# Kernel tuning notes

Hardware: AMD Instinct MI355X
Metric: run time of the kernel (lower is better)

Reference implementation:

```python
import jax, jax.numpy as jnp
import numpy as np

N_EV, N_CS, N_TR, N_ENV = 40000, 30000, 20000, 10000
N = N_EV + N_CS + N_TR + N_ENV  # 100000 nodes
E = 3_200_000                   # edges (avg degree 32)
FEAT, HID = 32, 64
N_GRAPHS, NPG = 100, 1000       # 100 graphs of 1000 nodes


def _p(k, shape, scale=0.1):
    return (jax.random.normal(k, shape, jnp.float32) * scale)


def setup_inputs() -> dict:
    key = jax.random.key(0)
    ks = jax.random.split(key, 24)
    inp = {
        'ev_features': jax.random.normal(ks[0], (N_EV, 6), jnp.float32),
        'cs_features': jax.random.normal(ks[1], (N_CS, 4), jnp.float32),
        'tr_features': jax.random.normal(ks[2], (N_TR, 2), jnp.float32),
        'env_features': jax.random.normal(ks[3], (N_ENV, 5), jnp.float32),
        'edge_index': jax.random.randint(ks[4], (2, E), 0, N, jnp.int32),
        'ev_indexes': jnp.arange(0, N_EV, dtype=jnp.int32),
        'cs_indexes': jnp.arange(N_EV, N_EV + N_CS, dtype=jnp.int32),
        'tr_indexes': jnp.arange(N_EV + N_CS, N_EV + N_CS + N_TR, dtype=jnp.int32),
        'env_indexes': jnp.arange(N - N_ENV, N, dtype=jnp.int32),
        'batch': (jnp.arange(N, dtype=jnp.int32) // NPG),
        'W_ev': _p(ks[5], (6, FEAT)),  'b_ev': _p(ks[6], (FEAT,)),
        'W_cs': _p(ks[7], (4, FEAT)),  'b_cs': _p(ks[8], (FEAT,)),
        'W_tr': _p(ks[9], (2, FEAT)),  'b_tr': _p(ks[10], (FEAT,)),
        'W_env': _p(ks[11], (5, FEAT)), 'b_env': _p(ks[12], (FEAT,)),
        'W1': _p(ks[13], (FEAT, HID)),      'b1': _p(ks[14], (HID,)),
        'W2': _p(ks[15], (HID, 2 * HID)),   'b2': _p(ks[16], (2 * HID,)),
        'W3': _p(ks[17], (2 * HID, HID)),   'b3': _p(ks[18], (HID,)),
    }
    return inp


def gcn_conv(x, src, dst, W, b):
    # PyG GCNConv: h = x W; add self-loops; symmetric norm D^-1/2 (A+I) D^-1/2; + bias
    h = x @ W
    ones_e = jnp.ones((src.shape[0],), h.dtype)
    deg = jnp.ones((N,), h.dtype).at[dst].add(ones_e)  # includes self-loop weight 1
    dinv = jax.lax.rsqrt(deg)
    norm = dinv[src] * dinv[dst]                       # [E]
    out = (h * (dinv * dinv)[:, None]).at[dst].add(h[src] * norm[:, None])
    return out + b


def reference(ev_features, cs_features, tr_features, env_features,
              edge_index, ev_indexes, cs_indexes, tr_indexes, env_indexes, batch,
              W_ev, b_ev, W_cs, b_cs, W_tr, b_tr, W_env, b_env,
              W1, b1, W2, b2, W3, b3):
    src, dst = edge_index[0], edge_index[1]
    x = jnp.zeros((N, FEAT), jnp.float32)
    x = x.at[ev_indexes].set(ev_features @ W_ev + b_ev)
    x = x.at[cs_indexes].set(cs_features @ W_cs + b_cs)
    x = x.at[tr_indexes].set(tr_features @ W_tr + b_tr)
    x = x.at[env_indexes].set(env_features @ W_env + b_env)

    x1 = gcn_conv(x, src, dst, W1, b1)                 # [N, HID]
    h = jax.nn.relu(x1)
    h = jax.nn.relu(gcn_conv(h, src, dst, W2, b2))     # [N, 2*HID]
    h = jax.nn.relu(gcn_conv(h, src, dst, W3, b3))     # [N, HID]
    h = h + x1                                          # residual

    # global_mean_pool over graph segments
    sums = jax.ops.segment_sum(h, batch, num_segments=N_GRAPHS)
    cnts = jax.ops.segment_sum(jnp.ones((N,), h.dtype), batch, num_segments=N_GRAPHS)
    return sums / cnts[:, None]
```

## Files before the change

### kernel.cpp

```cpp
#include <hip/hip_runtime.h>
#include <hip/hip_bf16.h>


#define THREADS 256
#define BINSHIFT 8
#define EPBA 4096
#define SCANCH 8

typedef __attribute__((ext_vector_type(8))) short short8;
typedef __attribute__((ext_vector_type(4))) float f32x4;

__device__ __forceinline__ unsigned bfpack2(float lo, float hi) {
    unsigned ul = __float_as_uint(lo);
    unsigned uh = __float_as_uint(hi);
    ul = (ul + 0x7fffu + ((ul >> 16) & 1u)) >> 16;
    uh = (uh + 0x7fffu + ((uh >> 16) & 1u)) & 0xffff0000u;
    return ul | uh;
}

__device__ __forceinline__ void bfacc(uint2 v, float& a0, float& a1,
                                      float& a2, float& a3) {
    a0 += __uint_as_float(v.x << 16);
    a1 += __uint_as_float(v.x & 0xffff0000u);
    a2 += __uint_as_float(v.y << 16);
    a3 += __uint_as_float(v.y & 0xffff0000u);
}

__device__ __forceinline__ short8 as_short8(uint4 u) {
    union { uint4 u; short8 s; } c; c.u = u; return c.s;
}

__global__ __launch_bounds__(THREADS)
void k_partcnt(const int* __restrict__ dst, int* __restrict__ counts,
               int nblk_part, int nb, int e) {
    extern __shared__ int h[];
    int t = threadIdx.x;
    for (int i = t; i < nb; i += THREADS) h[i] = 0;
    __syncthreads();
    int lo = blockIdx.x * EPBA;
    int hi = min(lo + EPBA, e);
    for (int i = lo + t; i < hi; i += THREADS)
        atomicAdd(&h[dst[i] >> BINSHIFT], 1);
    __syncthreads();
    for (int i = t; i < nb; i += THREADS)
        counts[(size_t)i * nblk_part + blockIdx.x] = h[i];
}

__global__ __launch_bounds__(THREADS)
void k_scanrows(int* __restrict__ counts, int* __restrict__ bintot, int nblk_part) {
    __shared__ int wsum[THREADS];
    int* row = counts + (size_t)blockIdx.x * nblk_part;
    int t = threadIdx.x;
    int base = t * SCANCH;
    int v[SCANCH];
    int s = 0;
#pragma unroll
    for (int k = 0; k < SCANCH; ++k) {
        v[k] = (base + k < nblk_part) ? row[base + k] : 0;
        s += v[k];
    }
    wsum[t] = s;
    __syncthreads();
    for (int off = 1; off < THREADS; off <<= 1) {
        int a = (t >= off) ? wsum[t - off] : 0;
        __syncthreads();
        wsum[t] += a;
        __syncthreads();
    }
    int run = wsum[t] - s;
#pragma unroll
    for (int k = 0; k < SCANCH; ++k) {
        int c = v[k];
        if (base + k < nblk_part) row[base + k] = run;
        run += c;
    }
    if (t == THREADS - 1) bintot[blockIdx.x] = run;
}

__global__ __launch_bounds__(512)
void k_binscan(const int* __restrict__ bintot, int* __restrict__ binptr,
               int nb, int e) {
    __shared__ int lds[512];
    int t = threadIdx.x;
    int v = (t < nb) ? bintot[t] : 0;
    lds[t] = v;
    __syncthreads();
    for (int off = 1; off < 512; off <<= 1) {
        int a = (t >= off) ? lds[t - off] : 0;
        __syncthreads();
        lds[t] += a;
        __syncthreads();
    }
    if (t < nb) binptr[t] = lds[t] - v;
    if (t == 0) binptr[nb] = e;
}

__global__ __launch_bounds__(THREADS)
void k_partwrite(const int* __restrict__ src, const int* __restrict__ dst,
                 const int* __restrict__ binptr, const int* __restrict__ counts,
                 int nblk_part, unsigned* __restrict__ pairs, int nb, int e) {
    extern __shared__ int smem[];
    int* base = smem;
    int* cnt  = smem + nb;
    int t = threadIdx.x;
    for (int i = t; i < nb; i += THREADS) {
        base[i] = binptr[i] + counts[(size_t)i * nblk_part + blockIdx.x];
        cnt[i] = 0;
    }
    __syncthreads();
    int lo = blockIdx.x * EPBA;
    int hi = min(lo + EPBA, e);
    for (int i = lo + t; i < hi; i += THREADS) {
        int s = src[i], d = dst[i];
        int b = d >> BINSHIFT;
        int pos = atomicAdd(&cnt[b], 1);
        pairs[base[b] + pos] = ((unsigned)s << BINSHIFT) | (unsigned)(d & ((1 << BINSHIFT) - 1));
    }
}

__global__ __launch_bounds__(THREADS)
void k_bincsr(const unsigned* __restrict__ pairs, const int* __restrict__ binptr,
              int* __restrict__ rowptr, float* __restrict__ dinv,
              int* __restrict__ srcs, int n, int nb, int e) {
    __shared__ int lcnt[256];
    __shared__ int lofs[256];
    int b = blockIdx.x, t = threadIdx.x;
    int e0 = binptr[b], e1 = binptr[b + 1];
    int n0 = b << BINSHIFT;
    constexpr unsigned NMASK = (1u << BINSHIFT) - 1u;
    lcnt[t] = 0;
    __syncthreads();
    for (int j = e0 + t; j < e1; j += THREADS)
        atomicAdd(&lcnt[pairs[j] & NMASK], 1);
    __syncthreads();
    int c = lcnt[t];
    lofs[t] = c;
    __syncthreads();
    for (int off = 1; off < THREADS; off <<= 1) {
        int a = (t >= off) ? lofs[t - off] : 0;
        __syncthreads();
        lofs[t] += a;
        __syncthreads();
    }
    int excl = lofs[t] - c;
    __syncthreads();
    lofs[t] = excl;
    int node = n0 + t;
    if (node < n) {
        rowptr[node] = e0 + excl;
        dinv[node] = rsqrtf((float)c + 1.0f);
    }
    if (b == nb - 1 && t == 0) rowptr[n] = e;
    __syncthreads();
    for (int j = e0 + t; j < e1; j += THREADS) {
        unsigned pp = pairs[j];
        int pos = e0 + atomicAdd(&lofs[pp & NMASK], 1);
        srcs[pos] = (int)(pp >> BINSHIFT);
    }
}

template <int K>
__global__ __launch_bounds__(THREADS)
void k_embed(const float* __restrict__ f, const float* __restrict__ W,
             const float* __restrict__ b, const int* __restrict__ idx,
             const float* __restrict__ dinv, int rows, unsigned* __restrict__ xb) {
    int g = blockIdx.x * THREADS + threadIdx.x;
    int r = g >> 4, cp = g & 15;
    if (r >= rows) return;
    int node = idx[r];
    float dv = dinv[node];
    float a0 = b[2 * cp], a1 = b[2 * cp + 1];
#pragma unroll
    for (int k = 0; k < K; ++k) {
        float fv = f[r * K + k];
        a0 += fv * W[k * 32 + 2 * cp];
        a1 += fv * W[k * 32 + 2 * cp + 1];
    }
    xb[(size_t)node * 16 + cp] = bfpack2(dv * a0, dv * a1);
}

template <bool HASBIAS, bool OUTRELU, bool HASRES, bool OUTBF>
__global__ __launch_bounds__(THREADS)
void k_gather64(const unsigned* __restrict__ tblb, const int* __restrict__ rowptr,
                const int* __restrict__ srcs, const float* __restrict__ dinv,
                const float* __restrict__ bias, const unsigned* __restrict__ resid,
                void* __restrict__ outp, int n) {
    int gt = blockIdx.x * THREADS + threadIdx.x;
    int node = gt >> 6;
    int lane = threadIdx.x & 63;
    if (node >= n) return;
    int qw = lane >> 4, li = lane & 15;
    const uint2* t2 = reinterpret_cast<const uint2*>(tblb);
    float a0 = 0.f, a1 = 0.f, a2 = 0.f, a3 = 0.f;
    int beg = rowptr[node], end = rowptr[node + 1];
    int j = beg;
    for (; j + 16 <= end; j += 16) {
        int i0 = srcs[j + qw];
        int i1 = srcs[j + 4 + qw];
        int i2 = srcs[j + 8 + qw];
        int i3 = srcs[j + 12 + qw];
        uint2 v0 = t2[(size_t)i0 * 16 + li];
        uint2 v1 = t2[(size_t)i1 * 16 + li];
        uint2 v2 = t2[(size_t)i2 * 16 + li];
        uint2 v3 = t2[(size_t)i3 * 16 + li];
        bfacc(v0, a0, a1, a2, a3);
        bfacc(v1, a0, a1, a2, a3);
        bfacc(v2, a0, a1, a2, a3);
        bfacc(v3, a0, a1, a2, a3);
    }
    for (; j + 8 <= end; j += 8) {
        int i0 = srcs[j + qw];
        int i1 = srcs[j + 4 + qw];
        uint2 v0 = t2[(size_t)i0 * 16 + li];
        uint2 v1 = t2[(size_t)i1 * 16 + li];
        bfacc(v0, a0, a1, a2, a3);
        bfacc(v1, a0, a1, a2, a3);
    }
    int rem = end - j;
    if (qw < rem) {
        uint2 v = t2[(size_t)srcs[j + qw] * 16 + li];
        bfacc(v, a0, a1, a2, a3);
    }
    if (qw + 4 < rem) {
        uint2 v = t2[(size_t)srcs[j + 4 + qw] * 16 + li];
        bfacc(v, a0, a1, a2, a3);
    }
    a0 += __shfl_down(a0, 32, 64); a1 += __shfl_down(a1, 32, 64);
    a2 += __shfl_down(a2, 32, 64); a3 += __shfl_down(a3, 32, 64);
    a0 += __shfl_down(a0, 16, 64); a1 += __shfl_down(a1, 16, 64);
    a2 += __shfl_down(a2, 16, 64); a3 += __shfl_down(a3, 16, 64);
    if (lane < 16) {
        uint2 sv = t2[(size_t)node * 16 + li];
        bfacc(sv, a0, a1, a2, a3);
        float dv = dinv[node];
        float r0 = dv * a0, r1 = dv * a1, r2 = dv * a2, r3 = dv * a3;
        if (HASBIAS) {
            float4 bv = *reinterpret_cast<const float4*>(bias + 4 * li);
            r0 += bv.x; r1 += bv.y; r2 += bv.z; r3 += bv.w;
        }
        if (OUTRELU) {
            r0 = fmaxf(r0, 0.f); r1 = fmaxf(r1, 0.f);
            r2 = fmaxf(r2, 0.f); r3 = fmaxf(r3, 0.f);
        }
        if (HASRES) {
            uint2 rv = reinterpret_cast<const uint2*>(resid)[(size_t)node * 16 + li];
            bfacc(rv, r0, r1, r2, r3);
        }
        if (OUTBF) {
            uint2 o = {bfpack2(r0, r1), bfpack2(r2, r3)};
            reinterpret_cast<uint2*>(outp)[(size_t)node * 16 + li] = o;
        } else {
            float4 o = {r0, r1, r2, r3};
            reinterpret_cast<float4*>(outp)[(size_t)node * 16 + li] = o;
        }
    }
}

__global__ __launch_bounds__(THREADS)
void k_gather32(const unsigned* __restrict__ tblb, const int* __restrict__ rowptr,
                const int* __restrict__ srcs, const float* __restrict__ dinv,
                unsigned* __restrict__ outb, int n) {
    int gt = blockIdx.x * THREADS + threadIdx.x;
    int node = gt >> 6;
    int lane = threadIdx.x & 63;
    if (node >= n) return;
    int og = lane >> 3, li = lane & 7;
    const uint2* t2 = reinterpret_cast<const uint2*>(tblb);
    float a0 = 0.f, a1 = 0.f, a2 = 0.f, a3 = 0.f;
    int beg = rowptr[node], end = rowptr[node + 1];
    int j = beg;
    for (; j + 16 <= end; j += 16) {
        int i0 = srcs[j + og];
        int i1 = srcs[j + 8 + og];
        uint2 v0 = t2[(size_t)i0 * 8 + li];
        uint2 v1 = t2[(size_t)i1 * 8 + li];
        bfacc(v0, a0, a1, a2, a3);
        bfacc(v1, a0, a1, a2, a3);
    }
    for (; j + 8 <= end; j += 8) {
        int i0 = srcs[j + og];
        uint2 v0 = t2[(size_t)i0 * 8 + li];
        bfacc(v0, a0, a1, a2, a3);
    }
    int rem = end - j;
    if (og < rem) {
        uint2 v = t2[(size_t)srcs[j + og] * 8 + li];
        bfacc(v, a0, a1, a2, a3);
    }
    a0 += __shfl_down(a0, 32, 64); a1 += __shfl_down(a1, 32, 64);
    a2 += __shfl_down(a2, 32, 64); a3 += __shfl_down(a3, 32, 64);
    a0 += __shfl_down(a0, 16, 64); a1 += __shfl_down(a1, 16, 64);
    a2 += __shfl_down(a2, 16, 64); a3 += __shfl_down(a3, 16, 64);
    a0 += __shfl_down(a0, 8, 64);  a1 += __shfl_down(a1, 8, 64);
    a2 += __shfl_down(a2, 8, 64);  a3 += __shfl_down(a3, 8, 64);
    if (lane < 8) {
        uint2 sv = t2[(size_t)node * 8 + li];
        bfacc(sv, a0, a1, a2, a3);
        float dv = dinv[node];
        uint2 o = {bfpack2(dv * a0, dv * a1), bfpack2(dv * a2, dv * a3)};
        reinterpret_cast<uint2*>(outb)[(size_t)node * 8 + li] = o;
    }
}

template <int FIN, int FOUT>
__global__ __launch_bounds__(THREADS)
void k_wprep(const float* __restrict__ W, unsigned* __restrict__ Wtb) {
    int g = blockIdx.x * THREADS + threadIdx.x;
    if (g >= FOUT * (FIN / 2)) return;
    int nn = g / (FIN / 2), kq = g % (FIN / 2);
    float lo = W[(size_t)(2 * kq) * FOUT + nn];
    float hi = W[(size_t)(2 * kq + 1) * FOUT + nn];
    Wtb[g] = bfpack2(lo, hi);
}

template <int FIN, int FOUT, int EXTRA>
__global__ __launch_bounds__(THREADS)
void k_mmfa(const unsigned* __restrict__ xinb, const unsigned* __restrict__ wtb,
            const float* __restrict__ bias, const float* __restrict__ dinv,
            unsigned* __restrict__ outb, unsigned* __restrict__ outb2, int nrows) {
    constexpr int FH = FIN / 2;
    constexpr int KS = FIN / 32;
    constexpr int MT = FOUT / 16;
    int tid = threadIdx.x;
    int lane = tid & 63;
    int lg = lane >> 4, li = lane & 15;
    int node = blockIdx.x * 64 + (tid >> 6) * 16 + li;
    int nc = min(node, nrows - 1);

    const uint4* xr = reinterpret_cast<const uint4*>(xinb + (size_t)nc * FH);
    short8 bf[KS];
#pragma unroll
    for (int ks = 0; ks < KS; ++ks) bf[ks] = as_short8(xr[ks * 4 + lg]);

    f32x4 acc[MT];
#pragma unroll
    for (int mt = 0; mt < MT; ++mt) acc[mt] = (f32x4){0.f, 0.f, 0.f, 0.f};

#pragma unroll
    for (int ks = 0; ks < KS; ++ks) {
#pragma unroll
        for (int mt = 0; mt < MT; ++mt) {
            uint4 wu = *reinterpret_cast<const uint4*>(
                wtb + (size_t)(mt * 16 + li) * FH + ks * 16 + lg * 4);
            acc[mt] = __builtin_amdgcn_mfma_f32_16x16x32_bf16(
                as_short8(wu), bf[ks], acc[mt], 0, 0, 0);
        }
    }

    if (node >= nrows) return;
    float dv = (EXTRA != 3) ? dinv[node] : 0.f;
#pragma unroll
    for (int mt = 0; mt < MT; ++mt) {
        float v0 = acc[mt][0], v1 = acc[mt][1], v2 = acc[mt][2], v3 = acc[mt][3];
        int m0 = mt * 16 + lg * 4;
        if (EXTRA == 1 || EXTRA == 3) {
            float4 bv = *reinterpret_cast<const float4*>(bias + m0);
            v0 += bv.x; v1 += bv.y; v2 += bv.z; v3 += bv.w;
        }
        size_t ob = (size_t)node * (FOUT / 2) + mt * 8 + lg * 2;
        if (EXTRA == 1) {
            uint2 o = {bfpack2(v0, v1), bfpack2(v2, v3)};
            *reinterpret_cast<uint2*>(outb + ob) = o;
            uint2 s = {bfpack2(dv * fmaxf(v0, 0.f), dv * fmaxf(v1, 0.f)),
                       bfpack2(dv * fmaxf(v2, 0.f), dv * fmaxf(v3, 0.f))};
            *reinterpret_cast<uint2*>(outb2 + ob) = s;
        }
        if (EXTRA == 3) {
            uint2 o = {bfpack2(fmaxf(v0, 0.f), fmaxf(v1, 0.f)),
                       bfpack2(fmaxf(v2, 0.f), fmaxf(v3, 0.f))};
            *reinterpret_cast<uint2*>(outb + ob) = o;
        }
        if (EXTRA == 2) {
            uint2 o = {bfpack2(dv * v0, dv * v1), bfpack2(dv * v2, dv * v3)};
            *reinterpret_cast<uint2*>(outb + ob) = o;
        }
    }
}

__global__ __launch_bounds__(THREADS)
void k_pool(const float* __restrict__ h, const int* __restrict__ batch,
            float* __restrict__ sums, float* __restrict__ cnts, int n) {
    int c = threadIdx.x & 63;
    int rq = threadIdx.x >> 6;
    int r0 = blockIdx.x * THREADS;
    int rend = min(r0 + THREADS, n);
    int curg = -1;
    float acc = 0.f, cacc = 0.f;
    for (int r = r0 + rq; r < rend; r += 4) {
        int g = batch[r];
        if (g != curg) {
            if (curg >= 0) {
                atomicAdd(&sums[(size_t)curg * 64 + c], acc);
                if (c == 0) atomicAdd(&cnts[curg], cacc);
            }
            curg = g; acc = 0.f; cacc = 0.f;
        }
        acc += h[(size_t)r * 64 + c];
        cacc += 1.f;
    }
    if (curg >= 0) {
        atomicAdd(&sums[(size_t)curg * 64 + c], acc);
        if (c == 0) atomicAdd(&cnts[curg], cacc);
    }
}

__global__ __launch_bounds__(THREADS)
void k_div(const float* __restrict__ sums, const float* __restrict__ cnts,
           float* __restrict__ out, int total) {
    int i = blockIdx.x * THREADS + threadIdx.x;
    if (i < total) out[i] = sums[i] / cnts[i >> 6];
}

static inline size_t alignup(size_t v) { return (v + 255) & ~(size_t)255; }

extern "C" void kernel_launch(void* const* d_in, const int* in_sizes, int n_in,
                              void* d_out, int out_size, void* d_ws, size_t ws_size,
                              hipStream_t stream) {
    const float* ev_f  = (const float*)d_in[0];
    const float* cs_f  = (const float*)d_in[1];
    const float* tr_f  = (const float*)d_in[2];
    const float* env_f = (const float*)d_in[3];
    const int*   ei    = (const int*)d_in[4];
    const int*   ev_i  = (const int*)d_in[5];
    const int*   cs_i  = (const int*)d_in[6];
    const int*   tr_i  = (const int*)d_in[7];
    const int*   env_i = (const int*)d_in[8];
    const int*   batch = (const int*)d_in[9];
    const float* W_ev = (const float*)d_in[10]; const float* b_ev = (const float*)d_in[11];
    const float* W_cs = (const float*)d_in[12]; const float* b_cs = (const float*)d_in[13];
    const float* W_tr = (const float*)d_in[14]; const float* b_tr = (const float*)d_in[15];
    const float* W_env= (const float*)d_in[16]; const float* b_env= (const float*)d_in[17];
    const float* W1 = (const float*)d_in[18]; const float* b1 = (const float*)d_in[19];
    const float* W2 = (const float*)d_in[20]; const float* b2 = (const float*)d_in[21];
    const float* W3 = (const float*)d_in[22]; const float* b3 = (const float*)d_in[23];

    const int E_ = in_sizes[4] / 2;
    const int N_ = in_sizes[9];
    const int n_ev  = in_sizes[5];
    const int n_cs  = in_sizes[6];
    const int n_tr  = in_sizes[7];
    const int n_env = in_sizes[8];
    const int ngr   = out_size / 64;

    const int* e_src = ei;
    const int* e_dst = ei + E_;

    const int NB   = (N_ + (1 << BINSHIFT) - 1) >> BINSHIFT;
    const int ablk = (E_ + EPBA - 1) / EPBA;

    char* p = (char*)d_ws;
    int*      counts = (int*)p;      p += alignup((size_t)NB * ablk * 4);
    int*      bintot = (int*)p;      p += alignup((size_t)NB * 4);
    int*      binptr = (int*)p;      p += alignup(((size_t)NB + 1) * 4);
    int*      rowptr = (int*)p;      p += alignup(((size_t)N_ + 1) * 4);
    float*    dinv   = (float*)p;    p += alignup((size_t)N_ * 4);
    int*      srcs   = (int*)p;      p += alignup((size_t)E_ * 4);
    unsigned* xb     = (unsigned*)p; p += alignup((size_t)N_ * 16 * 4);
    unsigned* x1b    = (unsigned*)p; p += alignup((size_t)N_ * 32 * 4);
    unsigned* x1s_bf = (unsigned*)p; p += alignup((size_t)N_ * 32 * 4);
    unsigned* aggb   = (unsigned*)p; p += alignup((size_t)N_ * 32 * 4);
    unsigned* hA     = (unsigned*)p; p += alignup((size_t)N_ * 64 * 4);
    unsigned* t3s_bf = (unsigned*)p; p += alignup((size_t)N_ * 32 * 4);
    float*    hfin   = (float*)p;    p += alignup((size_t)N_ * 64 * 4);
    unsigned* w1t    = (unsigned*)p; p += alignup((size_t)64 * 16 * 4);
    unsigned* w2t    = (unsigned*)p; p += alignup((size_t)128 * 32 * 4);
    unsigned* w3t    = (unsigned*)p; p += alignup((size_t)64 * 64 * 4);
    float*    sums   = (float*)p;    p += alignup((size_t)ngr * 64 * 4);
    float*    cnts   = (float*)p;    p += alignup((size_t)ngr * 4);

    unsigned* pairs = hA;

    const int nblk  = (N_ + THREADS - 1) / THREADS;
    const int mfblk = (N_ + 63) / 64;
    const int gblk  = ((size_t)N_ * 64 + THREADS - 1) / THREADS;

    hipMemsetAsync(sums, 0, (size_t)ngr * 64 * 4, stream);
    hipMemsetAsync(cnts, 0, (size_t)ngr * 4, stream);

    k_partcnt<<<ablk, THREADS, (size_t)NB * 4, stream>>>(e_dst, counts, ablk, NB, E_);
    k_scanrows<<<NB, THREADS, 0, stream>>>(counts, bintot, ablk);
    k_binscan<<<1, 512, 0, stream>>>(bintot, binptr, NB, E_);
    k_partwrite<<<ablk, THREADS, (size_t)NB * 8, stream>>>(e_src, e_dst, binptr, counts, ablk, pairs, NB, E_);
    k_bincsr<<<NB, THREADS, 0, stream>>>(pairs, binptr, rowptr, dinv, srcs, N_, NB, E_);

    k_wprep<32, 64><<<(64 * 16 + THREADS - 1) / THREADS, THREADS, 0, stream>>>(W1, w1t);
    k_wprep<64, 128><<<(128 * 32 + THREADS - 1) / THREADS, THREADS, 0, stream>>>(W2, w2t);
    k_wprep<128, 64><<<(64 * 64 + THREADS - 1) / THREADS, THREADS, 0, stream>>>(W3, w3t);

    k_embed<6><<<((size_t)n_ev  * 16 + THREADS - 1) / THREADS, THREADS, 0, stream>>>(ev_f,  W_ev,  b_ev,  ev_i,  dinv, n_ev,  xb);
    k_embed<4><<<((size_t)n_cs  * 16 + THREADS - 1) / THREADS, THREADS, 0, stream>>>(cs_f,  W_cs,  b_cs,  cs_i,  dinv, n_cs,  xb);
    k_embed<2><<<((size_t)n_tr  * 16 + THREADS - 1) / THREADS, THREADS, 0, stream>>>(tr_f,  W_tr,  b_tr,  tr_i,  dinv, n_tr,  xb);
    k_embed<5><<<((size_t)n_env * 16 + THREADS - 1) / THREADS, THREADS, 0, stream>>>(env_f, W_env, b_env, env_i, dinv, n_env, xb);

    k_gather32<<<gblk, THREADS, 0, stream>>>(xb, rowptr, srcs, dinv, aggb, N_);
    k_mmfa<32, 64, 1><<<mfblk, THREADS, 0, stream>>>(aggb, w1t, b1, dinv, x1b, x1s_bf, N_);

    k_gather64<false, false, false, true><<<gblk, THREADS, 0, stream>>>(
        x1s_bf, rowptr, srcs, dinv, nullptr, nullptr, aggb, N_);
    k_mmfa<64, 128, 3><<<mfblk, THREADS, 0, stream>>>(aggb, w2t, b2, nullptr, hA, nullptr, N_);

    k_mmfa<128, 64, 2><<<mfblk, THREADS, 0, stream>>>(hA, w3t, nullptr, dinv, t3s_bf, nullptr, N_);
    k_gather64<true, true, true, false><<<gblk, THREADS, 0, stream>>>(
        t3s_bf, rowptr, srcs, dinv, b3, x1b, hfin, N_);

    k_pool<<<nblk, THREADS, 0, stream>>>(hfin, batch, sums, cnts, N_);
    k_div<<<(out_size + THREADS - 1) / THREADS, THREADS, 0, stream>>>(sums, cnts, (float*)d_out, out_size);
}
```

Baseline: 361.0 us.

## Merge embed and weight-prep launches, deepen gather unroll, pool from bf16 output

The four per-type embedding kernels become one launch driven by a struct of pointers and cumulative row offsets. The three weight-transpose kernels become one launch. Both gather kernels now issue 8 or 4 independent row loads per iteration instead of 4 or 2, to keep more memory requests in flight. The final gather writes bf16 instead of fp32 and the pooling kernel reads it, which halves that intermediate traffic but rounds the pooled input to bf16.

After: 359.4 us. Within noise of the previous version (-0.4%).

```diff
diff --git a/kernel.cpp b/kernel.cpp
--- a/kernel.cpp
+++ b/kernel.cpp
@@ -159,18 +159,30 @@
     }
 }
 
-template <int K>
-__global__ __launch_bounds__(THREADS)
-void k_embed(const float* __restrict__ f, const float* __restrict__ W,
-             const float* __restrict__ b, const int* __restrict__ idx,
-             const float* __restrict__ dinv, int rows, unsigned* __restrict__ xb) {
+struct EmbedArgs {
+    const float* f[4];
+    const float* W[4];
+    const float* b[4];
+    const int*   idx[4];
+    int cum[5];
+    int Kv[4];
+};
+
+__global__ __launch_bounds__(THREADS)
+void k_embed_all(EmbedArgs ea, const float* __restrict__ dinv,
+                 unsigned* __restrict__ xb) {
     int g = blockIdx.x * THREADS + threadIdx.x;
-    int r = g >> 4, cp = g & 15;
-    if (r >= rows) return;
-    int node = idx[r];
+    int row = g >> 4, cp = g & 15;
+    if (row >= ea.cum[4]) return;
+    int t = (row >= ea.cum[1]) + (row >= ea.cum[2]) + (row >= ea.cum[3]);
+    int r = row - ea.cum[t];
+    int K = ea.Kv[t];
+    const float* f  = ea.f[t];
+    const float* W  = ea.W[t];
+    const float* bb = ea.b[t];
+    int node = ea.idx[t][r];
     float dv = dinv[node];
-    float a0 = b[2 * cp], a1 = b[2 * cp + 1];
-#pragma unroll
+    float a0 = bb[2 * cp], a1 = bb[2 * cp + 1];
     for (int k = 0; k < K; ++k) {
         float fv = f[r * K + k];
         a0 += fv * W[k * 32 + 2 * cp];
@@ -194,25 +206,21 @@
     float a0 = 0.f, a1 = 0.f, a2 = 0.f, a3 = 0.f;
     int beg = rowptr[node], end = rowptr[node + 1];
     int j = beg;
-    for (; j + 16 <= end; j += 16) {
-        int i0 = srcs[j + qw];
-        int i1 = srcs[j + 4 + qw];
-        int i2 = srcs[j + 8 + qw];
-        int i3 = srcs[j + 12 + qw];
-        uint2 v0 = t2[(size_t)i0 * 16 + li];
-        uint2 v1 = t2[(size_t)i1 * 16 + li];
-        uint2 v2 = t2[(size_t)i2 * 16 + li];
-        uint2 v3 = t2[(size_t)i3 * 16 + li];
-        bfacc(v0, a0, a1, a2, a3);
-        bfacc(v1, a0, a1, a2, a3);
-        bfacc(v2, a0, a1, a2, a3);
-        bfacc(v3, a0, a1, a2, a3);
+    for (; j + 32 <= end; j += 32) {
+        int s[8];
+#pragma unroll
+        for (int u = 0; u < 8; ++u) s[u] = srcs[j + 4 * u + qw];
+        uint2 v[8];
+#pragma unroll
+        for (int u = 0; u < 8; ++u) v[u] = t2[(size_t)s[u] * 16 + li];
+#pragma unroll
+        for (int u = 0; u < 8; ++u) bfacc(v[u], a0, a1, a2, a3);
     }
     for (; j + 8 <= end; j += 8) {
-        int i0 = srcs[j + qw];
-        int i1 = srcs[j + 4 + qw];
-        uint2 v0 = t2[(size_t)i0 * 16 + li];
-        uint2 v1 = t2[(size_t)i1 * 16 + li];
+        int s0 = srcs[j + qw];
+        int s1 = srcs[j + 4 + qw];
+        uint2 v0 = t2[(size_t)s0 * 16 + li];
+        uint2 v1 = t2[(size_t)s1 * 16 + li];
         bfacc(v0, a0, a1, a2, a3);
         bfacc(v1, a0, a1, a2, a3);
     }
@@ -269,17 +277,19 @@
     float a0 = 0.f, a1 = 0.f, a2 = 0.f, a3 = 0.f;
     int beg = rowptr[node], end = rowptr[node + 1];
     int j = beg;
-    for (; j + 16 <= end; j += 16) {
-        int i0 = srcs[j + og];
-        int i1 = srcs[j + 8 + og];
-        uint2 v0 = t2[(size_t)i0 * 8 + li];
-        uint2 v1 = t2[(size_t)i1 * 8 + li];
-        bfacc(v0, a0, a1, a2, a3);
-        bfacc(v1, a0, a1, a2, a3);
+    for (; j + 32 <= end; j += 32) {
+        int s[4];
+#pragma unroll
+        for (int u = 0; u < 4; ++u) s[u] = srcs[j + 8 * u + og];
+        uint2 v[4];
+#pragma unroll
+        for (int u = 0; u < 4; ++u) v[u] = t2[(size_t)s[u] * 8 + li];
+#pragma unroll
+        for (int u = 0; u < 4; ++u) bfacc(v[u], a0, a1, a2, a3);
     }
     for (; j + 8 <= end; j += 8) {
-        int i0 = srcs[j + og];
-        uint2 v0 = t2[(size_t)i0 * 8 + li];
+        int s0 = srcs[j + og];
+        uint2 v0 = t2[(size_t)s0 * 8 + li];
         bfacc(v0, a0, a1, a2, a3);
     }
     int rem = end - j;
@@ -302,15 +312,22 @@
     }
 }
 
-template <int FIN, int FOUT>
-__global__ __launch_bounds__(THREADS)
-void k_wprep(const float* __restrict__ W, unsigned* __restrict__ Wtb) {
+__global__ __launch_bounds__(THREADS)
+void k_wprep_all(const float* __restrict__ W1, const float* __restrict__ W2,
+                 const float* __restrict__ W3, unsigned* __restrict__ wt) {
     int g = blockIdx.x * THREADS + threadIdx.x;
-    if (g >= FOUT * (FIN / 2)) return;
-    int nn = g / (FIN / 2), kq = g % (FIN / 2);
-    float lo = W[(size_t)(2 * kq) * FOUT + nn];
-    float hi = W[(size_t)(2 * kq + 1) * FOUT + nn];
-    Wtb[g] = bfpack2(lo, hi);
+    if (g < 1024) {
+        int nn = g >> 4, kq = g & 15;
+        wt[g] = bfpack2(W1[(size_t)(2 * kq) * 64 + nn], W1[(size_t)(2 * kq + 1) * 64 + nn]);
+    } else if (g < 5120) {
+        int gg = g - 1024;
+        int nn = gg >> 5, kq = gg & 31;
+        wt[g] = bfpack2(W2[(size_t)(2 * kq) * 128 + nn], W2[(size_t)(2 * kq + 1) * 128 + nn]);
+    } else if (g < 9216) {
+        int gg = g - 5120;
+        int nn = gg >> 6, kq = gg & 63;
+        wt[g] = bfpack2(W3[(size_t)(2 * kq) * 64 + nn], W3[(size_t)(2 * kq + 1) * 64 + nn]);
+    }
 }
 
 template <int FIN, int FOUT, int EXTRA>
@@ -378,28 +395,32 @@
 }
 
 __global__ __launch_bounds__(THREADS)
-void k_pool(const float* __restrict__ h, const int* __restrict__ batch,
+void k_pool(const unsigned* __restrict__ hb, const int* __restrict__ batch,
             float* __restrict__ sums, float* __restrict__ cnts, int n) {
-    int c = threadIdx.x & 63;
-    int rq = threadIdx.x >> 6;
+    int c = threadIdx.x & 31;
+    int rq = threadIdx.x >> 5;
     int r0 = blockIdx.x * THREADS;
     int rend = min(r0 + THREADS, n);
     int curg = -1;
-    float acc = 0.f, cacc = 0.f;
-    for (int r = r0 + rq; r < rend; r += 4) {
+    float a0 = 0.f, a1 = 0.f, cacc = 0.f;
+    for (int r = r0 + rq; r < rend; r += 8) {
         int g = batch[r];
         if (g != curg) {
             if (curg >= 0) {
-                atomicAdd(&sums[(size_t)curg * 64 + c], acc);
+                atomicAdd(&sums[(size_t)curg * 64 + 2 * c], a0);
+                atomicAdd(&sums[(size_t)curg * 64 + 2 * c + 1], a1);
                 if (c == 0) atomicAdd(&cnts[curg], cacc);
             }
-            curg = g; acc = 0.f; cacc = 0.f;
-        }
-        acc += h[(size_t)r * 64 + c];
+            curg = g; a0 = 0.f; a1 = 0.f; cacc = 0.f;
+        }
+        unsigned u = hb[(size_t)r * 32 + c];
+        a0 += __uint_as_float(u << 16);
+        a1 += __uint_as_float(u & 0xffff0000u);
         cacc += 1.f;
     }
     if (curg >= 0) {
-        atomicAdd(&sums[(size_t)curg * 64 + c], acc);
+        atomicAdd(&sums[(size_t)curg * 64 + 2 * c], a0);
+        atomicAdd(&sums[(size_t)curg * 64 + 2 * c + 1], a1);
         if (c == 0) atomicAdd(&cnts[curg], cacc);
     }
 }
@@ -461,12 +482,14 @@
     unsigned* aggb   = (unsigned*)p; p += alignup((size_t)N_ * 32 * 4);
     unsigned* hA     = (unsigned*)p; p += alignup((size_t)N_ * 64 * 4);
     unsigned* t3s_bf = (unsigned*)p; p += alignup((size_t)N_ * 32 * 4);
-    float*    hfin   = (float*)p;    p += alignup((size_t)N_ * 64 * 4);
-    unsigned* w1t    = (unsigned*)p; p += alignup((size_t)64 * 16 * 4);
-    unsigned* w2t    = (unsigned*)p; p += alignup((size_t)128 * 32 * 4);
-    unsigned* w3t    = (unsigned*)p; p += alignup((size_t)64 * 64 * 4);
+    unsigned* hfb    = (unsigned*)p; p += alignup((size_t)N_ * 32 * 4);
+    unsigned* wt     = (unsigned*)p; p += alignup((size_t)9216 * 4);
     float*    sums   = (float*)p;    p += alignup((size_t)ngr * 64 * 4);
     float*    cnts   = (float*)p;    p += alignup((size_t)ngr * 4);
+
+    unsigned* w1t = wt;
+    unsigned* w2t = wt + 1024;
+    unsigned* w3t = wt + 5120;
 
     unsigned* pairs = hA;
 
@@ -483,14 +506,23 @@
     k_partwrite<<<ablk, THREADS, (size_t)NB * 8, stream>>>(e_src, e_dst, binptr, counts, ablk, pairs, NB, E_);
     k_bincsr<<<NB, THREADS, 0, stream>>>(pairs, binptr, rowptr, dinv, srcs, N_, NB, E_);
 
-    k_wprep<32, 64><<<(64 * 16 + THREADS - 1) / THREADS, THREADS, 0, stream>>>(W1, w1t);
-    k_wprep<64, 128><<<(128 * 32 + THREADS - 1) / THREADS, THREADS, 0, stream>>>(W2, w2t);
-    k_wprep<128, 64><<<(64 * 64 + THREADS - 1) / THREADS, THREADS, 0, stream>>>(W3, w3t);
-
-    k_embed<6><<<((size_t)n_ev  * 16 + THREADS - 1) / THREADS, THREADS, 0, stream>>>(ev_f,  W_ev,  b_ev,  ev_i,  dinv, n_ev,  xb);
-    k_embed<4><<<((size_t)n_cs  * 16 + THREADS - 1) / THREADS, THREADS, 0, stream>>>(cs_f,  W_cs,  b_cs,  cs_i,  dinv, n_cs,  xb);
-    k_embed<2><<<((size_t)n_tr  * 16 + THREADS - 1) / THREADS, THREADS, 0, stream>>>(tr_f,  W_tr,  b_tr,  tr_i,  dinv, n_tr,  xb);
-    k_embed<5><<<((size_t)n_env * 16 + THREADS - 1) / THREADS, THREADS, 0, stream>>>(env_f, W_env, b_env, env_i, dinv, n_env, xb);
+    k_wprep_all<<<(9216 + THREADS - 1) / THREADS, THREADS, 0, stream>>>(W1, W2, W3, wt);
+
+    EmbedArgs ea;
+    ea.f[0] = ev_f;  ea.f[1] = cs_f;  ea.f[2] = tr_f;  ea.f[3] = env_f;
+    ea.W[0] = W_ev;  ea.W[1] = W_cs;  ea.W[2] = W_tr;  ea.W[3] = W_env;
+    ea.b[0] = b_ev;  ea.b[1] = b_cs;  ea.b[2] = b_tr;  ea.b[3] = b_env;
+    ea.idx[0] = ev_i; ea.idx[1] = cs_i; ea.idx[2] = tr_i; ea.idx[3] = env_i;
+    ea.cum[0] = 0;
+    ea.cum[1] = n_ev;
+    ea.cum[2] = n_ev + n_cs;
+    ea.cum[3] = n_ev + n_cs + n_tr;
+    ea.cum[4] = n_ev + n_cs + n_tr + n_env;
+    ea.Kv[0] = in_sizes[0] / n_ev;
+    ea.Kv[1] = in_sizes[1] / n_cs;
+    ea.Kv[2] = in_sizes[2] / n_tr;
+    ea.Kv[3] = in_sizes[3] / n_env;
+    k_embed_all<<<((size_t)ea.cum[4] * 16 + THREADS - 1) / THREADS, THREADS, 0, stream>>>(ea, dinv, xb);
 
     k_gather32<<<gblk, THREADS, 0, stream>>>(xb, rowptr, srcs, dinv, aggb, N_);
     k_mmfa<32, 64, 1><<<mfblk, THREADS, 0, stream>>>(aggb, w1t, b1, dinv, x1b, x1s_bf, N_);
@@ -500,9 +532,9 @@
     k_mmfa<64, 128, 3><<<mfblk, THREADS, 0, stream>>>(aggb, w2t, b2, nullptr, hA, nullptr, N_);
 
     k_mmfa<128, 64, 2><<<mfblk, THREADS, 0, stream>>>(hA, w3t, nullptr, dinv, t3s_bf, nullptr, N_);
-    k_gather64<true, true, true, false><<<gblk, THREADS, 0, stream>>>(
-        t3s_bf, rowptr, srcs, dinv, b3, x1b, hfin, N_);
-
-    k_pool<<<nblk, THREADS, 0, stream>>>(hfin, batch, sums, cnts, N_);
+    k_gather64<true, true, true, true><<<gblk, THREADS, 0, stream>>>(
+        t3s_bf, rowptr, srcs, dinv, b3, x1b, hfb, N_);
+
+    k_pool<<<nblk, THREADS, 0, stream>>>(hfb, batch, sums, cnts, N_);
     k_div<<<(out_size + THREADS - 1) / THREADS, THREADS, 0, stream>>>(sums, cnts, (float*)d_out, out_size);
 }
```
